# Kernel tuning notes

Hardware: AMD Instinct MI355X
Metric: run time of the kernel (lower is better)

Reference implementation:

```python
import jax, jax.numpy as jnp
import numpy as np

B, I, O = 32768, 512, 512
EPS = 1e-5


def setup_inputs() -> dict:
    key = jax.random.key(0)
    ks = jax.random.split(key, 4)
    return {
        "input": jax.random.normal(ks[0], (B, I), dtype=jnp.float32),
        "h": jax.random.normal(ks[1], (B, O), dtype=jnp.float32),
        "c": jax.random.normal(ks[2], (B, O), dtype=jnp.float32),
        "W": jax.random.normal(ks[3], (4 * O, I + O), dtype=jnp.float32) * (1.0 / np.sqrt(I + O)),
        "gamma": jnp.ones((4, O), dtype=jnp.float32),
        "beta": jnp.zeros((4, O), dtype=jnp.float32),
    }


def reference(input, h, c, W, gamma, beta):
    # fused input projection: [B, I+O] @ [I+O, 4O] -> [B, 4, O]
    z = jnp.einsum("bi,gi->bg", jnp.concatenate([input, h], axis=-1), W)
    z = z.reshape(z.shape[0], 4, O)
    # LayerNorm over the trailing [4, O] dims jointly (torch LayerNorm([x, o_size]))
    mean = jnp.mean(z, axis=(-2, -1), keepdims=True)
    var = jnp.var(z, axis=(-2, -1), keepdims=True)
    zn = (z - mean) * jax.lax.rsqrt(var + EPS) * gamma + beta
    f_gate = jax.nn.sigmoid(zn[:, 0])
    i_gate = jax.nn.sigmoid(zn[:, 1])
    o_gate = jax.nn.sigmoid(zn[:, 2])
    # GELU (torch default = exact erf); dropout is identity in eval mode
    h_state = jax.nn.gelu(zn[:, 3], approximate=False)
    cell = f_gate * c + i_gate * h_state
    output = o_gate * cell
    return (output, cell)
```

## Files before the change

kernel.cpp:

```cpp
#include <hip/hip_runtime.h>
#include <hip/hip_bf16.h>
#include <cstdint>
#include <cstddef>

#define BDIM 32768
#define IDIM 512
#define ODIM 512
#define KDIM 1024
#define NDIM 2048

typedef __attribute__((ext_vector_type(8))) __bf16 bf16x8;
typedef __attribute__((ext_vector_type(4))) float f32x4;
typedef __attribute__((ext_vector_type(8))) unsigned short u16x8;

__device__ __forceinline__ unsigned short f2bf(float x) {
  union { float f; uint32_t u; } v; v.f = x;
  uint32_t r = v.u + 0x7FFFu + ((v.u >> 16) & 1u);
  return (unsigned short)(r >> 16);
}

__device__ __forceinline__ float bf2f(unsigned short s) {
  union { uint32_t u; float f; } v; v.u = ((uint32_t)s) << 16;
  return v.f;
}


__global__ __launch_bounds__(256) void pack_a_kernel(const float* __restrict__ in,
                                                     const float* __restrict__ h,
                                                     unsigned short* __restrict__ A) {
  size_t t = (size_t)blockIdx.x * 256 + threadIdx.x;
  size_t e = t * 8;
  size_t b = e >> 10;
  int col = (int)(e & 1023);
  const float* src = (col < IDIM) ? (in + b * IDIM + col)
                                  : (h + b * ODIM + (col - IDIM));
  float4 v0 = ((const float4*)src)[0];
  float4 v1 = ((const float4*)src)[1];
  u16x8 r;
  r[0] = f2bf(v0.x); r[1] = f2bf(v0.y); r[2] = f2bf(v0.z); r[3] = f2bf(v0.w);
  r[4] = f2bf(v1.x); r[5] = f2bf(v1.y); r[6] = f2bf(v1.z); r[7] = f2bf(v1.w);
  *(u16x8*)(A + e) = r;
}

__global__ __launch_bounds__(256) void pack_w_kernel(const float* __restrict__ Wsrc,
                                                     unsigned short* __restrict__ Wb) {
  size_t t = (size_t)blockIdx.x * 256 + threadIdx.x;
  size_t e = t * 8;
  float4 v0 = ((const float4*)(Wsrc + e))[0];
  float4 v1 = ((const float4*)(Wsrc + e))[1];
  u16x8 r;
  r[0] = f2bf(v0.x); r[1] = f2bf(v0.y); r[2] = f2bf(v0.z); r[3] = f2bf(v0.w);
  r[4] = f2bf(v1.x); r[5] = f2bf(v1.y); r[6] = f2bf(v1.z); r[7] = f2bf(v1.w);
  *(u16x8*)(Wb + e) = r;
}


#define BUFSZ 32768

#define BAR() do { asm volatile("" ::: "memory"); __builtin_amdgcn_s_barrier(); asm volatile("" ::: "memory"); } while (0)
#define VMW(n) asm volatile("s_waitcnt vmcnt(" #n ")" ::: "memory")

__device__ __forceinline__ void gll16(const unsigned short* src, char* ldsdst) {
  __builtin_amdgcn_global_load_lds(
      (const __attribute__((address_space(1))) void*)src,
      (__attribute__((address_space(3))) void*)ldsdst, 16, 0, 0);
}

template<int BUF, int VM, bool STG>
__device__ __forceinline__ void ktile(char* smem, const char* aR, const char* bR,
                                      const unsigned short* pA0, const unsigned short* pA1,
                                      const unsigned short* pB0, const unsigned short* pB1,
                                      int stOff, f32x4 (&acc)[8][4]) {
  constexpr int CB = BUF * BUFSZ;
  constexpr int DB = ((BUF + 3) & 3) * BUFSZ;

  if (VM == 8)      VMW(8);
  else if (VM == 4) VMW(4);
  else              VMW(0);
  BAR();

  bf16x8 a0[4], qf[4], a1[4];
#pragma unroll
  for (int i = 0; i < 4; ++i) a0[i] = *(const bf16x8*)(aR + CB + i * 1024);
#pragma unroll
  for (int j = 0; j < 4; ++j) qf[j] = *(const bf16x8*)(bR + CB + j * 1024);
  if (STG) {
    gll16(pA0, smem + DB + stOff);
    gll16(pA1, smem + DB + 8192 + stOff);
  }
  BAR();
  __builtin_amdgcn_sched_barrier(0);
  __builtin_amdgcn_s_setprio(1);
#pragma unroll
  for (int i = 0; i < 4; ++i)
#pragma unroll
    for (int j = 0; j < 4; ++j)
      acc[i][j] = __builtin_amdgcn_mfma_f32_16x16x32_bf16(a0[i], qf[j], acc[i][j], 0, 0, 0);
  __builtin_amdgcn_s_setprio(0);
  __builtin_amdgcn_sched_barrier(0);
  BAR();

#pragma unroll
  for (int i = 0; i < 4; ++i) a1[i] = *(const bf16x8*)(aR + CB + (4 + i) * 1024);
  if (STG) {
    gll16(pB0, smem + DB + 16384 + stOff);
    gll16(pB1, smem + DB + 24576 + stOff);
  }
  BAR();
  __builtin_amdgcn_sched_barrier(0);
  __builtin_amdgcn_s_setprio(1);
#pragma unroll
  for (int i = 0; i < 4; ++i)
#pragma unroll
    for (int j = 0; j < 4; ++j)
      acc[4 + i][j] = __builtin_amdgcn_mfma_f32_16x16x32_bf16(a1[i], qf[j], acc[4 + i][j], 0, 0, 0);
  __builtin_amdgcn_s_setprio(0);
  __builtin_amdgcn_sched_barrier(0);
}

__global__ __launch_bounds__(512, 2) void gemm_kernel(const unsigned short* __restrict__ A,
                                                      const unsigned short* __restrict__ Bt,
                                                      unsigned short* __restrict__ Cz) {
  extern __shared__ char smem[];
  const int tid = threadIdx.x;
  const int w = tid >> 6;
  const int lane = tid & 63;

  const int bid = blockIdx.x;
  const int swz = (bid & 7) * 128 + (bid >> 3);
  const int m0 = (swz >> 3) * 256;
  const int n0 = (swz & 7) * 256;

  const int wm = (w >> 2) * 128;
  const int wn = (w & 3) * 64;
  const int lrow = lane & 15;
  const int lk = (lane >> 4) * 8;

  const char* aR = smem + (w >> 2) * 8192 + lane * 16;
  const char* bR = smem + 16384 + (w & 3) * 4096 + lane * 16;
  const int stOff = w * 1024 + lane * 16;

  const unsigned short* pA0 = A  + (size_t)(m0 + w * 16       + lrow) * KDIM + lk;
  const unsigned short* pA1 = A  + (size_t)(m0 + (8 + w) * 16 + lrow) * KDIM + lk;
  const unsigned short* pB0 = Bt + (size_t)(n0 + w * 16       + lrow) * KDIM + lk;
  const unsigned short* pB1 = Bt + (size_t)(n0 + (8 + w) * 16 + lrow) * KDIM + lk;

  f32x4 acc[8][4] = {};

#pragma unroll
  for (int t = 0; t < 3; ++t) {
    gll16(pA0 + t * 32, smem + t * BUFSZ + stOff);
    gll16(pA1 + t * 32, smem + t * BUFSZ + 8192 + stOff);
    gll16(pB0 + t * 32, smem + t * BUFSZ + 16384 + stOff);
    gll16(pB1 + t * 32, smem + t * BUFSZ + 24576 + stOff);
  }
  pA0 += 96; pA1 += 96; pB0 += 96; pB1 += 96;

  for (int tt = 0; tt < 7; ++tt) {
    ktile<0, 8, true>(smem, aR, bR, pA0, pA1, pB0, pB1, stOff, acc);
    pA0 += 32; pA1 += 32; pB0 += 32; pB1 += 32;
    ktile<1, 8, true>(smem, aR, bR, pA0, pA1, pB0, pB1, stOff, acc);
    pA0 += 32; pA1 += 32; pB0 += 32; pB1 += 32;
    ktile<2, 8, true>(smem, aR, bR, pA0, pA1, pB0, pB1, stOff, acc);
    pA0 += 32; pA1 += 32; pB0 += 32; pB1 += 32;
    ktile<3, 8, true>(smem, aR, bR, pA0, pA1, pB0, pB1, stOff, acc);
    pA0 += 32; pA1 += 32; pB0 += 32; pB1 += 32;
  }
  ktile<0, 8, true >(smem, aR, bR, pA0, pA1, pB0, pB1, stOff, acc);
  ktile<1, 8, false>(smem, aR, bR, pA0, pA1, pB0, pB1, stOff, acc);
  ktile<2, 4, false>(smem, aR, bR, pA0, pA1, pB0, pB1, stOff, acc);
  ktile<3, 0, false>(smem, aR, bR, pA0, pA1, pB0, pB1, stOff, acc);

#pragma unroll
  for (int mi = 0; mi < 8; ++mi) {
#pragma unroll
    for (int ni = 0; ni < 4; ++ni) {
#pragma unroll
      for (int r = 0; r < 4; ++r) {
        const int row = m0 + wm + mi * 16 + (lane >> 4) * 4 + r;
        const int col = n0 + wn + ni * 16 + lrow;
        Cz[(size_t)row * NDIM + col] = f2bf(acc[mi][ni][r]);
      }
    }
  }
}


__global__ __launch_bounds__(256) void ln_gate_kernel(const unsigned short* __restrict__ z,
                                                      const float* __restrict__ c,
                                                      const float* __restrict__ gamma,
                                                      const float* __restrict__ beta,
                                                      float* __restrict__ out) {
  __shared__ float rowbuf[4][NDIM];
  const int wave = threadIdx.x >> 6;
  const int lane = threadIdx.x & 63;
  const int row = blockIdx.x * 4 + wave;
  const unsigned short* zr = z + (size_t)row * NDIM;

  float s = 0.f, ss = 0.f;
#pragma unroll
  for (int j = 0; j < 4; ++j) {
    const int chunk = j * 64 + lane;
    u16x8 v = *(const u16x8*)(zr + chunk * 8);
    float f[8];
#pragma unroll
    for (int i2 = 0; i2 < 8; ++i2) {
      f[i2] = bf2f(v[i2]);
      s += f[i2];
      ss += f[i2] * f[i2];
    }
    float4* dst = (float4*)&rowbuf[wave][chunk * 8];
    dst[0] = make_float4(f[0], f[1], f[2], f[3]);
    dst[1] = make_float4(f[4], f[5], f[6], f[7]);
  }
#pragma unroll
  for (int off = 32; off > 0; off >>= 1) {
    s += __shfl_xor(s, off, 64);
    ss += __shfl_xor(ss, off, 64);
  }
  const float mean = s * (1.f / (float)NDIM);
  const float var = ss * (1.f / (float)NDIM) - mean * mean;
  const float inv = rsqrtf(var + 1e-5f);

  float* out_o = out + (size_t)row * ODIM;
  float* out_c = out + (size_t)BDIM * ODIM + (size_t)row * ODIM;
  const float* crow = c + (size_t)row * ODIM;

#pragma unroll
  for (int j = 0; j < 8; ++j) {
    const int o = j * 64 + lane;
    float zn[4];
#pragma unroll
    for (int g = 0; g < 4; ++g) {
      float v = (rowbuf[wave][g * ODIM + o] - mean) * inv;
      zn[g] = v * gamma[g * ODIM + o] + beta[g * ODIM + o];
    }
    const float fg = 1.f / (1.f + expf(-zn[0]));
    const float ig = 1.f / (1.f + expf(-zn[1]));
    const float og = 1.f / (1.f + expf(-zn[2]));
    const float x = zn[3];
    const float hs = 0.5f * x * (1.f + erff(x * 0.70710678118654752f));
    const float cc = fg * crow[o] + ig * hs;
    out_c[o] = cc;
    out_o[o] = og * cc;
  }
}


extern "C" void kernel_launch(void* const* d_in, const int* in_sizes, int n_in,
                              void* d_out, int out_size, void* d_ws, size_t ws_size,
                              hipStream_t stream) {
  const float* input = (const float*)d_in[0];
  const float* h     = (const float*)d_in[1];
  const float* c     = (const float*)d_in[2];
  const float* W     = (const float*)d_in[3];
  const float* gamma = (const float*)d_in[4];
  const float* beta  = (const float*)d_in[5];

  unsigned short* A  = (unsigned short*)d_ws;
  unsigned short* Wb = A + (size_t)BDIM * KDIM;
  unsigned short* z  = Wb + (size_t)NDIM * KDIM;
  float* out = (float*)d_out;

  hipFuncSetAttribute((const void*)gemm_kernel,
                      hipFuncAttributeMaxDynamicSharedMemorySize, 131072);

  pack_a_kernel<<<(BDIM * KDIM / 8) / 256, 256, 0, stream>>>(input, h, A);
  pack_w_kernel<<<(NDIM * KDIM / 8) / 256, 256, 0, stream>>>(W, Wb);
  gemm_kernel<<<dim3((BDIM / 256) * (NDIM / 256)), 512, 131072, stream>>>(A, Wb, z);
  ln_gate_kernel<<<BDIM / 4, 256, 0, stream>>>(z, c, gamma, beta, out);
}
```

Measured before the change: 286.5 us.

## Switch GEMM from 4-stage to double-buffered LDS pipeline to halve shared memory

```diff
diff --git a/kernel.cpp b/kernel.cpp
--- a/kernel.cpp
+++ b/kernel.cpp
@@ -59,6 +59,7 @@
 
 #define BAR() do { asm volatile("" ::: "memory"); __builtin_amdgcn_s_barrier(); asm volatile("" ::: "memory"); } while (0)
 #define VMW(n) asm volatile("s_waitcnt vmcnt(" #n ")" ::: "memory")
+#define LGKM0() do { asm volatile("s_waitcnt lgkmcnt(0)" ::: "memory"); __builtin_amdgcn_sched_barrier(0); } while (0)
 
 __device__ __forceinline__ void gll16(const unsigned short* src, char* ldsdst) {
   __builtin_amdgcn_global_load_lds(
@@ -66,54 +67,50 @@
       (__attribute__((address_space(3))) void*)ldsdst, 16, 0, 0);
 }
 
-template<int BUF, int VM, bool STG>
-__device__ __forceinline__ void ktile(char* smem, const char* aR, const char* bR,
-                                      const unsigned short* pA0, const unsigned short* pA1,
-                                      const unsigned short* pB0, const unsigned short* pB1,
-                                      int stOff, f32x4 (&acc)[8][4]) {
-  constexpr int CB = BUF * BUFSZ;
-  constexpr int DB = ((BUF + 3) & 3) * BUFSZ;
-
-  if (VM == 8)      VMW(8);
-  else if (VM == 4) VMW(4);
-  else              VMW(0);
+template<int CBUF, bool STG>
+__device__ __forceinline__ void ktile32(char* smem, const char* aRd, const char* bRd,
+                                        const unsigned short* pA0, const unsigned short* pA1,
+                                        const unsigned short* pB0, const unsigned short* pB1,
+                                        int stOff, f32x4 (&acc)[8][4]) {
+  constexpr int CB = CBUF * BUFSZ;
+  constexpr int SB = (CBUF ^ 1) * BUFSZ;
+  bf16x8 a[4], qf[4];
+
+  VMW(0);
   BAR();
 
-  bf16x8 a0[4], qf[4], a1[4];
-#pragma unroll
-  for (int i = 0; i < 4; ++i) a0[i] = *(const bf16x8*)(aR + CB + i * 1024);
-#pragma unroll
-  for (int j = 0; j < 4; ++j) qf[j] = *(const bf16x8*)(bR + CB + j * 1024);
+#pragma unroll
+  for (int i = 0; i < 4; ++i) a[i] = *(const bf16x8*)(aRd + CB + i * 1024);
+#pragma unroll
+  for (int j = 0; j < 4; ++j) qf[j] = *(const bf16x8*)(bRd + CB + j * 1024);
   if (STG) {
-    gll16(pA0, smem + DB + stOff);
-    gll16(pA1, smem + DB + 8192 + stOff);
-  }
-  BAR();
-  __builtin_amdgcn_sched_barrier(0);
+    gll16(pA0, smem + SB + stOff);
+    gll16(pA1, smem + SB + 8192 + stOff);
+  }
+  BAR(); LGKM0();
   __builtin_amdgcn_s_setprio(1);
 #pragma unroll
   for (int i = 0; i < 4; ++i)
 #pragma unroll
     for (int j = 0; j < 4; ++j)
-      acc[i][j] = __builtin_amdgcn_mfma_f32_16x16x32_bf16(a0[i], qf[j], acc[i][j], 0, 0, 0);
+      acc[i][j] = __builtin_amdgcn_mfma_f32_16x16x32_bf16(a[i], qf[j], acc[i][j], 0, 0, 0);
   __builtin_amdgcn_s_setprio(0);
   __builtin_amdgcn_sched_barrier(0);
   BAR();
 
 #pragma unroll
-  for (int i = 0; i < 4; ++i) a1[i] = *(const bf16x8*)(aR + CB + (4 + i) * 1024);
+  for (int i = 0; i < 4; ++i) a[i] = *(const bf16x8*)(aRd + CB + (4 + i) * 1024);
   if (STG) {
-    gll16(pB0, smem + DB + 16384 + stOff);
-    gll16(pB1, smem + DB + 24576 + stOff);
-  }
-  BAR();
-  __builtin_amdgcn_sched_barrier(0);
+    gll16(pB0, smem + SB + 16384 + stOff);
+    gll16(pB1, smem + SB + 24576 + stOff);
+  }
+  BAR(); LGKM0();
   __builtin_amdgcn_s_setprio(1);
 #pragma unroll
   for (int i = 0; i < 4; ++i)
 #pragma unroll
     for (int j = 0; j < 4; ++j)
-      acc[4 + i][j] = __builtin_amdgcn_mfma_f32_16x16x32_bf16(a1[i], qf[j], acc[4 + i][j], 0, 0, 0);
+      acc[4 + i][j] = __builtin_amdgcn_mfma_f32_16x16x32_bf16(a[i], qf[j], acc[4 + i][j], 0, 0, 0);
   __builtin_amdgcn_s_setprio(0);
   __builtin_amdgcn_sched_barrier(0);
 }
@@ -136,8 +133,8 @@
   const int lrow = lane & 15;
   const int lk = (lane >> 4) * 8;
 
-  const char* aR = smem + (w >> 2) * 8192 + lane * 16;
-  const char* bR = smem + 16384 + (w & 3) * 4096 + lane * 16;
+  const char* aRd = smem + (w >> 2) * 8192 + lane * 16;
+  const char* bRd = smem + 16384 + (w & 3) * 4096 + lane * 16;
   const int stOff = w * 1024 + lane * 16;
 
   const unsigned short* pA0 = A  + (size_t)(m0 + w * 16       + lrow) * KDIM + lk;
@@ -147,29 +144,20 @@
 
   f32x4 acc[8][4] = {};
 
-#pragma unroll
-  for (int t = 0; t < 3; ++t) {
-    gll16(pA0 + t * 32, smem + t * BUFSZ + stOff);
-    gll16(pA1 + t * 32, smem + t * BUFSZ + 8192 + stOff);
-    gll16(pB0 + t * 32, smem + t * BUFSZ + 16384 + stOff);
-    gll16(pB1 + t * 32, smem + t * BUFSZ + 24576 + stOff);
-  }
-  pA0 += 96; pA1 += 96; pB0 += 96; pB1 += 96;
-
-  for (int tt = 0; tt < 7; ++tt) {
-    ktile<0, 8, true>(smem, aR, bR, pA0, pA1, pB0, pB1, stOff, acc);
+  gll16(pA0, smem + stOff);
+  gll16(pA1, smem + 8192 + stOff);
+  gll16(pB0, smem + 16384 + stOff);
+  gll16(pB1, smem + 24576 + stOff);
+  pA0 += 32; pA1 += 32; pB0 += 32; pB1 += 32;
+
+  for (int tt = 0; tt < 15; ++tt) {
+    ktile32<0, true>(smem, aRd, bRd, pA0, pA1, pB0, pB1, stOff, acc);
     pA0 += 32; pA1 += 32; pB0 += 32; pB1 += 32;
-    ktile<1, 8, true>(smem, aR, bR, pA0, pA1, pB0, pB1, stOff, acc);
+    ktile32<1, true>(smem, aRd, bRd, pA0, pA1, pB0, pB1, stOff, acc);
     pA0 += 32; pA1 += 32; pB0 += 32; pB1 += 32;
-    ktile<2, 8, true>(smem, aR, bR, pA0, pA1, pB0, pB1, stOff, acc);
-    pA0 += 32; pA1 += 32; pB0 += 32; pB1 += 32;
-    ktile<3, 8, true>(smem, aR, bR, pA0, pA1, pB0, pB1, stOff, acc);
-    pA0 += 32; pA1 += 32; pB0 += 32; pB1 += 32;
-  }
-  ktile<0, 8, true >(smem, aR, bR, pA0, pA1, pB0, pB1, stOff, acc);
-  ktile<1, 8, false>(smem, aR, bR, pA0, pA1, pB0, pB1, stOff, acc);
-  ktile<2, 4, false>(smem, aR, bR, pA0, pA1, pB0, pB1, stOff, acc);
-  ktile<3, 0, false>(smem, aR, bR, pA0, pA1, pB0, pB1, stOff, acc);
+  }
+  ktile32<0, true >(smem, aRd, bRd, pA0, pA1, pB0, pB1, stOff, acc);
+  ktile32<1, false>(smem, aRd, bRd, pA0, pA1, pB0, pB1, stOff, acc);
 
 #pragma unroll
   for (int mi = 0; mi < 8; ++mi) {
@@ -263,10 +251,10 @@
   float* out = (float*)d_out;
 
   hipFuncSetAttribute((const void*)gemm_kernel,
-                      hipFuncAttributeMaxDynamicSharedMemorySize, 131072);
+                      hipFuncAttributeMaxDynamicSharedMemorySize, 65536);
 
   pack_a_kernel<<<(BDIM * KDIM / 8) / 256, 256, 0, stream>>>(input, h, A);
   pack_w_kernel<<<(NDIM * KDIM / 8) / 256, 256, 0, stream>>>(W, Wb);
-  gemm_kernel<<<dim3((BDIM / 256) * (NDIM / 256)), 512, 131072, stream>>>(A, Wb, z);
+  gemm_kernel<<<dim3((BDIM / 256) * (NDIM / 256)), 512, 65536, stream>>>(A, Wb, z);
   ln_gate_kernel<<<BDIM / 4, 256, 0, stream>>>(z, c, gamma, beta, out);
 }
```

Measured after the change: 301.9 us. 5.4% more time.
